# Performance work log

Measured on AMD Instinct MI355X. Metric: run time of the kernel, lower is better.

## Reference

```python
import jax, jax.numpy as jnp
import numpy as np

K = 20  # knn neighbors (module default)


def _edge_conv(h, W, s, b):
    # h: [P, C] point features; W: [O, 2C] 1x1 conv weight; s,b: folded BN scale/shift [O]
    g = h @ h.T                                   # [P, P] inner products
    sq = jnp.sum(h * h, axis=-1)                  # [P]
    pd = 2.0 * g - sq[:, None] - sq[None, :]      # negative squared distance (torch knn)
    idx = jax.lax.top_k(pd, K)[1]                 # [P, K] nearest (includes self)
    nb = h[idx]                                   # [P, K, C]
    ctr = jnp.broadcast_to(h[:, None, :], nb.shape)
    edge = jnp.concatenate([nb - ctr, ctr], axis=-1)   # [P, K, 2C]
    y = jnp.einsum('pkc,oc->pko', edge, W)        # 1x1 conv
    y = jax.nn.leaky_relu(y * s + b, 0.2)         # BN (eval, folded) + LeakyReLU
    return jnp.max(y, axis=1)                     # max over neighbors -> [P, O]


def setup_inputs() -> dict:
    key = jax.random.key(0)
    ks = list(jax.random.split(key, 40))
    N, C, B, P = 50000, 128, 16, 1024
    d = {}
    d['features'] = jax.random.normal(ks[0], (N, C), jnp.float32)
    d['clusters'] = jax.random.randint(ks[1], (B, P), 0, N)
    i = 2
    def mk_w(shape):
        nonlocal i
        w = jax.random.normal(ks[i], shape, jnp.float32) * 0.05; i += 1
        return w
    def mk_bn(c):
        nonlocal i
        s = jax.random.uniform(ks[i], (c,), jnp.float32, 0.5, 1.5); i += 1
        b = jax.random.normal(ks[i], (c,), jnp.float32) * 0.1; i += 1
        return s, b
    # EdgeConv blocks: (out, in=2*prev)
    d['W1'] = mk_w((64, 256));  d['s1'], d['b1'] = mk_bn(64)
    d['W2'] = mk_w((64, 128));  d['s2'], d['b2'] = mk_bn(64)
    d['W3'] = mk_w((128, 128)); d['s3'], d['b3'] = mk_bn(128)
    d['W4'] = mk_w((256, 256)); d['s4'], d['b4'] = mk_bn(256)
    d['W5'] = mk_w((512, 512)); d['s5'], d['b5'] = mk_bn(512)
    d['L1'] = mk_w((512, 1024)); d['s6'], d['b6'] = mk_bn(512)
    d['L2'] = mk_w((256, 512)); d['bl2'] = jax.random.normal(ks[i], (256,), jnp.float32) * 0.05; i += 1
    d['s7'], d['b7'] = mk_bn(256)
    d['L3'] = mk_w((1, 256));   d['bl3'] = jax.random.normal(ks[i], (1,), jnp.float32) * 0.05; i += 1
    return d


def reference(clusters, features, W1, s1, b1, W2, s2, b2, W3, s3, b3,
              W4, s4, b4, W5, s5, b5, L1, s6, b6, L2, bl2, s7, b7, L3, bl3):
    def _cluster(h):  # h: [P, 128]
        x1 = _edge_conv(h,  W1, s1, b1)   # [P, 64]
        x2 = _edge_conv(x1, W2, s2, b2)   # [P, 64]
        x3 = _edge_conv(x2, W3, s3, b3)   # [P, 128]
        x4 = _edge_conv(x3, W4, s4, b4)   # [P, 256]
        xc = jnp.concatenate([x1, x2, x3, x4], axis=-1)            # [P, 512]
        y = jax.nn.leaky_relu((xc @ W5.T) * s5 + b5, 0.2)          # conv5 + BN + lrelu
        return jnp.concatenate([jnp.max(y, 0), jnp.mean(y, 0)])    # [1024] max+avg pool

    feat = jax.vmap(_cluster)(features[clusters])                  # [B, 1024]
    z = jax.nn.leaky_relu((feat @ L1.T) * s6 + b6, 0.2)            # dropout = identity (eval)
    z = jax.nn.leaky_relu((z @ L2.T + bl2) * s7 + b7, 0.2)
    z = z @ L3.T + bl3
    return jax.nn.sigmoid(z)                                       # [B, 1]
```

## Files before the change

### kernel.cpp

```cpp
#include <hip/hip_runtime.h>
#include <math.h>

#define KNN 20
#define PPTS 1024
#define NCL 16

typedef _Float16 f16x8 __attribute__((ext_vector_type(8)));
typedef _Float16 f16x4 __attribute__((ext_vector_type(4)));
typedef float f32x4 __attribute__((ext_vector_type(4)));

__device__ __forceinline__ float lrelu(float x) { return x > 0.f ? x : 0.2f * x; }

#define DPPMAX(x, ctrl) { \
    unsigned _t = (unsigned)__builtin_amdgcn_update_dpp((int)(x), (int)(x), ctrl, 0xF, 0xF, false); \
    (x) = (x) > _t ? (x) : _t; }




__global__ void gather_kernel(const float4* __restrict__ feat,
                              const int* __restrict__ clusters,
                              f16x4* __restrict__ hf,
                              float* __restrict__ sqp) {
    int n = blockIdx.x * 256 + threadIdx.x;
    int c4 = n & 31;
    int row = n >> 5;
    int src = clusters[row];
    float4 v = feat[(size_t)src * 32 + c4];
    f16x4 o;
    o[0] = (_Float16)v.x; o[1] = (_Float16)v.y; o[2] = (_Float16)v.z; o[3] = (_Float16)v.w;
    hf[(size_t)(row >> 4) * 512 + (c4 >> 3) * 128 + (row & 15) * 8 + (c4 & 7)] = o;
    float s = v.x * v.x + v.y * v.y + v.z * v.z + v.w * v.w;
    #pragma unroll
    for (int off = 16; off; off >>= 1) s += __shfl_xor(s, off);
    if (c4 == 0) { sqp[2 * row] = s; sqp[2 * row + 1] = 0.f; }
}

__global__ void tof16_tiled_kernel(const float* __restrict__ src,
                                   f16x4* __restrict__ dst) {
    int n = blockIdx.x * 256 + threadIdx.x;
    int c4 = n & 127;
    int row = n >> 7;
    float4 v = *(const float4*)&src[(size_t)row * 512 + c4 * 4];
    f16x4 o;
    o[0] = (_Float16)v.x; o[1] = (_Float16)v.y; o[2] = (_Float16)v.z; o[3] = (_Float16)v.w;
    dst[(size_t)(row >> 4) * 2048 + (c4 >> 3) * 128 + (row & 15) * 8 + (c4 & 7)] = o;
}

__global__ void wcvt_kernel(const float* __restrict__ W, int lgC4,
                            f16x4* __restrict__ wn, f16x4* __restrict__ wv) {
    int n = blockIdx.x * 256 + threadIdx.x;
    int c4 = n & ((1 << lgC4) - 1);
    int o = n >> lgC4;
    int C = 4 << lgC4;
    float4 a = *(const float4*)&W[(size_t)o * 2 * C + c4 * 4];
    float4 b = *(const float4*)&W[(size_t)o * 2 * C + C + c4 * 4];
    f16x4 on, ov;
    on[0] = (_Float16)a.x; on[1] = (_Float16)a.y; on[2] = (_Float16)a.z; on[3] = (_Float16)a.w;
    ov[0] = (_Float16)(b.x - a.x); ov[1] = (_Float16)(b.y - a.y);
    ov[2] = (_Float16)(b.z - a.z); ov[3] = (_Float16)(b.w - a.w);
    size_t ti = (size_t)(o >> 4) * (C * 4) + (c4 >> 3) * 128 + (o & 15) * 8 + (c4 & 7);
    wn[ti] = on; wv[ti] = ov;
}

template<int C>
__global__ __launch_bounds__(1024, 8) void grampk_kernel(
    const _Float16* __restrict__ hf,
    const float* __restrict__ sqp, int* __restrict__ idx)
{
    __shared__ unsigned keys[16 * 1024];
    const int f = blockIdx.x;
    const int g = f >> 3;
    const int b = (f & 7) + 8 * (g >> 6);
    const int bxi = g & 63;
    const _Float16* hb = hf + (size_t)b * PPTS * C;
    const float* sqb = sqp + 2 * (b << 10);
    const int w = threadIdx.x >> 6;
    const int lane = threadIdx.x & 63;
    const int col16 = lane & 15, quad = lane >> 4;
    const int i0 = bxi * 16;
    const int j0 = w * 64;
    const _Float16* aB = hb + (size_t)bxi * 16 * C + col16 * 32 + quad * 8;
    const _Float16* bB = hb + (size_t)(w * 4) * 16 * C + col16 * 32 + quad * 8;
    f32x4 acc[4] = {};
    #pragma unroll
    for (int kc = 0; kc < C / 32; kc++) {
        f16x8 a = *(const f16x8*)&aB[kc * 512];
        #pragma unroll
        for (int t = 0; t < 4; t++) {
            f16x8 bf = *(const f16x8*)&bB[(size_t)t * 16 * C + kc * 512];
            acc[t] = __builtin_amdgcn_mfma_f32_16x16x32_f16(a, bf, acc[t], 0, 0, 0);
        }
    }
    #pragma unroll
    for (int t = 0; t < 4; t++) {
        int j = j0 + t * 16 + col16;
        float sqj = sqb[2 * j] + sqb[2 * j + 1];
        #pragma unroll
        for (int r = 0; r < 4; r++) {
            int row = quad * 4 + r;
            float val = __builtin_fmaf(2.f, acc[t][r], -sqj);
            unsigned u = __float_as_uint(val);
            unsigned key = (u & 0x80000000u) ? ~u : (u | 0x80000000u);
            keys[(row << 10) | ((j + 2 * row) & 1023)] = (key & 0xFFFFFC00u) | (unsigned)j;
        }
    }
    __syncthreads();
    {
        const int row = w;
        const unsigned* krow = &keys[row << 10];
        unsigned m1 = 0u, m2 = 0u, m3 = 0u;
        #pragma unroll
        for (int s = 0; s < 16; s++) {
            unsigned x = krow[s * 64 + lane];
            unsigned h1 = x > m1 ? x : m1, l1 = x < m1 ? x : m1;
            unsigned h2 = l1 > m2 ? l1 : m2, l2 = l1 < m2 ? l1 : m2;
            unsigned h3 = l2 > m3 ? l2 : m3;
            m1 = h1; m2 = h2; m3 = h3;
        }
        unsigned myout = 0;
        for (int kk = 0; kk < KNN; kk++) {
            unsigned x = m1;
            DPPMAX(x, 0xB1);
            DPPMAX(x, 0x4E);
            DPPMAX(x, 0x141);
            DPPMAX(x, 0x140);
            DPPMAX(x, 0x142);
            DPPMAX(x, 0x143);
            unsigned gm = (unsigned)__builtin_amdgcn_readlane((int)x, 63);
            if (lane == kk) myout = gm & 1023u;
            if (m1 == gm) {
                if (m2 != 0u) {
                    m1 = m2; m2 = m3; m3 = 0u;
                } else {
                    unsigned n1 = 0u, n2 = 0u, n3 = 0u;
                    #pragma unroll
                    for (int s = 0; s < 16; s++) {
                        unsigned x2 = krow[s * 64 + lane];
                        x2 = x2 < gm ? x2 : 0u;
                        unsigned h1 = x2 > n1 ? x2 : n1, l1 = x2 < n1 ? x2 : n1;
                        unsigned h2 = l1 > n2 ? l1 : n2, l2 = l1 < n2 ? l1 : n2;
                        unsigned h3 = l2 > n3 ? l2 : n3;
                        n1 = h1; n2 = h2; n3 = h3;
                    }
                    m1 = n1; m2 = n2; m3 = n3;
                }
            }
        }
        if (lane < KNN) idx[((size_t)b * PPTS + i0 + row) * KNN + lane] = (int)myout;
    }
}

template<int C>
__global__ __launch_bounds__(256, 4) void uv_mfma_kernel(
    const _Float16* __restrict__ hf, int lgO,
    const _Float16* __restrict__ wn, const _Float16* __restrict__ wv,
    float* __restrict__ U, float* __restrict__ V)
{
    constexpr int NBLK = 4 * (C / 32);
    __shared__ _Float16 nsh[NBLK * 640];
    __shared__ _Float16 vsh[NBLK * 640];
    const int O = 1 << lgO;
    const int f = blockIdx.x;
    const int r = f >> 3;
    const int c = (f & 7) + 8 * (r >> (lgO - 2));
    const int i2 = r & ((1 << (lgO - 2)) - 1);
    const int ox = i2 & ((O >> 6) - 1);
    const int yy = i2 >> (lgO - 6);
    const int w = threadIdx.x >> 6;
    const int lane = threadIdx.x & 63;
    const int col16 = lane & 15, quad = lane >> 4;
    const int r0 = (c * 16 + yy) * 64 + w * 16;
    const int o0 = ox * 64;
    const _Float16* aB = hf + (size_t)(r0 >> 4) * 16 * C + col16 * 32 + quad * 8;
    const _Float16* nS = wn + (size_t)(o0 >> 4) * 16 * C;
    const _Float16* vS = wv + (size_t)(o0 >> 4) * 16 * C;

    #pragma unroll
    for (int p = 0; p < C / 32; p++) {
        int h = (p * 256 + (int)threadIdx.x) * 8;
        int blk = h >> 9, col = (h >> 5) & 15, q = (h >> 3) & 3;
        int d = blk * 640 + col * 40 + q * 8;
        *(f16x8*)&nsh[d] = *(const f16x8*)&nS[h];
        *(f16x8*)&vsh[d] = *(const f16x8*)&vS[h];
    }
    __syncthreads();

    f32x4 au[4] = {}, av[4] = {};
    #pragma unroll
    for (int kc = 0; kc < C / 32; kc++) {
        f16x8 a = *(const f16x8*)&aB[kc * 512];
        #pragma unroll
        for (int t = 0; t < 4; t++) {
            int d = (t * (C / 32) + kc) * 640 + col16 * 40 + quad * 8;
            f16x8 bn = *(const f16x8*)&nsh[d];
            au[t] = __builtin_amdgcn_mfma_f32_16x16x32_f16(a, bn, au[t], 0, 0, 0);
            f16x8 bv = *(const f16x8*)&vsh[d];
            av[t] = __builtin_amdgcn_mfma_f32_16x16x32_f16(a, bv, av[t], 0, 0, 0);
        }
    }
    #pragma unroll
    for (int t = 0; t < 4; t++) {
        int o = o0 + t * 16 + col16;
        #pragma unroll
        for (int r2 = 0; r2 < 4; r2++) {
            int p = r0 + quad * 4 + r2;
            U[((size_t)p << lgO) + o] = au[t][r2];
            V[((size_t)p << lgO) + o] = av[t][r2];
        }
    }
}

__global__ void agg_kernel(const float* __restrict__ U, const float* __restrict__ V,
                           const int* __restrict__ idx, int lgO,
                           const float* __restrict__ sc, const float* __restrict__ bi,
                           _Float16* __restrict__ hnext,
                           _Float16* __restrict__ xcf, int co,
                           float* __restrict__ sqp)
{
    int O = 1 << lgO;
    int f = blockIdx.x;
    int rr = f >> 3;
    int c = (f & 7) + 8 * (rr >> (lgO + 2));
    int ii = rr & ((1 << (lgO + 2)) - 1);
    int n = (((c << (lgO + 2)) + ii) << 8) + threadIdx.x;
    int o = n & (O - 1);
    int pr = n >> lgO;
    int b = pr >> 10;
    const int* id = idx + (size_t)pr * KNN;
    float m = -INFINITY;
    #pragma unroll
    for (int k = 0; k < KNN; k++) {
        int j = id[k];
        float u = U[((size_t)(b * PPTS + j) << lgO) + o];
        m = fmaxf(m, u);
    }
    float val = lrelu((m + V[((size_t)pr << lgO) + o]) * sc[o] + bi[o]);
    _Float16 hv = (_Float16)val;
    int prg = pr >> 4, prr = pr & 15;
    xcf[(size_t)prg * 8192 + ((co + o) >> 5) * 512 + prr * 32 + (o & 31)] = hv;
    if (hnext) {
        hnext[(size_t)prg * 16 * O + (o >> 5) * 512 + prr * 32 + (o & 31)] = hv;
        float s = val * val;
        #pragma unroll
        for (int off = 32; off; off >>= 1) s += __shfl_xor(s, off);
        if ((threadIdx.x & 63) == 0) {
            sqp[2 * pr + ((o >> 6) & 1)] = s;
            if (lgO == 6) sqp[2 * pr + 1] = 0.f;
        }
    }
}

__global__ __launch_bounds__(256, 4) void conv5pool_kernel(
    const _Float16* __restrict__ xcf, const _Float16* __restrict__ w5f,
    const float* __restrict__ s5, const float* __restrict__ b5,
    float* __restrict__ pmax, float* __restrict__ psum)
{
    __shared__ _Float16 bsh[2][8 * 640];
    __shared__ float lmax[4][128], lsum[4][128];
    const int f = blockIdx.x;
    const int r = f >> 3;
    const int c = (f & 7) + 8 * (r >> 5);
    const int within = r & 31;
    const int pb = within >> 2;
    const int ob = within & 3;
    const int w = threadIdx.x >> 6;
    const int lane = threadIdx.x & 63;
    const int col16 = lane & 15, quad = lane >> 4;
    const int p0 = (c * 8 + pb) * 128 + w * 32;
    const int o0 = ob * 128;
    const _Float16* aB = xcf + (size_t)(p0 >> 4) * 8192 + col16 * 32 + quad * 8;
    const _Float16* bS = w5f + (size_t)(o0 >> 4) * 8192;

    auto stage = [&](int kc, int buf) {
        #pragma unroll
        for (int s = 0; s < 2; s++) {
            int h = (s * 256 + (int)threadIdx.x) * 8;
            int t = h >> 9, rr2 = (h >> 5) & 15, q = (h >> 3) & 3;
            f16x8 x = *(const f16x8*)&bS[(size_t)t * 8192 + kc * 512 + rr2 * 32 + q * 8];
            *(f16x8*)&bsh[buf][t * 640 + rr2 * 40 + q * 8] = x;
        }
    };

    stage(0, 0);
    f32x4 acc[2][8] = {};
    for (int kc = 0; kc < 16; kc++) {
        int cur = kc & 1;
        __syncthreads();
        if (kc < 15) stage(kc + 1, cur ^ 1);
        f16x8 a0 = *(const f16x8*)&aB[kc * 512];
        f16x8 a1 = *(const f16x8*)&aB[8192 + kc * 512];
        #pragma unroll
        for (int t = 0; t < 8; t++) {
            f16x8 bf = *(const f16x8*)&bsh[cur][t * 640 + col16 * 40 + quad * 8];
            acc[0][t] = __builtin_amdgcn_mfma_f32_16x16x32_f16(a0, bf, acc[0][t], 0, 0, 0);
            acc[1][t] = __builtin_amdgcn_mfma_f32_16x16x32_f16(a1, bf, acc[1][t], 0, 0, 0);
        }
    }
    #pragma unroll
    for (int t = 0; t < 8; t++) {
        int o = o0 + t * 16 + col16;
        float sc = s5[o], bi = b5[o];
        float vm = -INFINITY, vs = 0.f;
        #pragma unroll
        for (int u = 0; u < 2; u++)
            #pragma unroll
            for (int r2 = 0; r2 < 4; r2++) {
                float val = lrelu(acc[u][t][r2] * sc + bi);
                vm = fmaxf(vm, val); vs += val;
            }
        #pragma unroll
        for (int off = 16; off < 64; off <<= 1) {
            vm = fmaxf(vm, __shfl_xor(vm, off));
            vs += __shfl_xor(vs, off);
        }
        if (quad == 0) { lmax[w][t * 16 + col16] = vm; lsum[w][t * 16 + col16] = vs; }
    }
    __syncthreads();
    if (threadIdx.x < 128) {
        int col = threadIdx.x;
        float m = lmax[0][col], s = lsum[0][col];
        #pragma unroll
        for (int q = 1; q < 4; q++) { m = fmaxf(m, lmax[q][col]); s += lsum[q][col]; }
        size_t o = (size_t)(c * 8 + pb) * 512 + o0 + col;
        pmax[o] = m; psum[o] = s;
    }
}

__global__ void poolred_kernel(const float* __restrict__ pmax, const float* __restrict__ psum,
                               float* __restrict__ feat) {
    int n = blockIdx.x * 256 + threadIdx.x;
    int o = n & 511, cl = n >> 9;
    float m = -INFINITY, s = 0.f;
    #pragma unroll
    for (int c = 0; c < 8; c++) {
        size_t q = (size_t)(cl * 8 + c) * 512 + o;
        m = fmaxf(m, pmax[q]); s += psum[q];
    }
    feat[(size_t)cl * 1024 + o] = m;
    feat[(size_t)cl * 1024 + 512 + o] = s * (1.f / 1024.f);
}

__global__ void mlp1_kernel(const float* __restrict__ feat, const float* __restrict__ L1,
                            const float* __restrict__ s6, const float* __restrict__ b6,
                            float* __restrict__ z1) {
    int wid = (blockIdx.x * 256 + threadIdx.x) >> 6;
    int lane = threadIdx.x & 63;
    int o = wid & 511, b = wid >> 9;
    const float* f = feat + (size_t)b * 1024;
    const float* w = L1 + (size_t)o * 1024;
    float acc = 0.f;
    #pragma unroll
    for (int i = 0; i < 16; i++) acc = fmaf(f[i * 64 + lane], w[i * 64 + lane], acc);
    #pragma unroll
    for (int off = 32; off; off >>= 1) acc += __shfl_xor(acc, off);
    if (lane == 0) z1[wid] = lrelu(acc * s6[o] + b6[o]);
}

__global__ void mlp2_kernel(const float* __restrict__ z1, const float* __restrict__ L2,
                            const float* __restrict__ bl2,
                            const float* __restrict__ s7, const float* __restrict__ b7,
                            float* __restrict__ z2) {
    int wid = (blockIdx.x * 256 + threadIdx.x) >> 6;
    int lane = threadIdx.x & 63;
    int o = wid & 255, b = wid >> 8;
    const float* f = z1 + (size_t)b * 512;
    const float* w = L2 + (size_t)o * 512;
    float acc = 0.f;
    #pragma unroll
    for (int i = 0; i < 8; i++) acc = fmaf(f[i * 64 + lane], w[i * 64 + lane], acc);
    #pragma unroll
    for (int off = 32; off; off >>= 1) acc += __shfl_xor(acc, off);
    if (lane == 0) z2[wid] = lrelu((acc + bl2[o]) * s7[o] + b7[o]);
}

__global__ void mlp3_kernel(const float* __restrict__ z2, const float* __restrict__ L3,
                            const float* __restrict__ bl3, float* __restrict__ out) {
    __shared__ float red[256];
    int t = threadIdx.x;
    int b = t >> 4, q = t & 15;
    float acc = 0.f;
    for (int c = q * 16; c < q * 16 + 16; c++) acc = fmaf(z2[(size_t)b * 256 + c], L3[c], acc);
    red[t] = acc;
    __syncthreads();
    if (q == 0) {
        float s = 0.f;
        #pragma unroll
        for (int i = 0; i < 16; i++) s += red[b * 16 + i];
        s += bl3[0];
        out[b] = 1.f / (1.f + expf(-s));
    }
}

extern "C" void kernel_launch(void* const* d_in, const int* in_sizes, int n_in,
                              void* d_out, int out_size, void* d_ws, size_t ws_size,
                              hipStream_t stream) {
    const float* features = (const float*)d_in[0];
    const int*   clusters = (const int*)d_in[1];
    const float* W1 = (const float*)d_in[2];
    const float* s1 = (const float*)d_in[3];
    const float* b1 = (const float*)d_in[4];
    const float* W2 = (const float*)d_in[5];
    const float* s2 = (const float*)d_in[6];
    const float* b2 = (const float*)d_in[7];
    const float* W3 = (const float*)d_in[8];
    const float* s3 = (const float*)d_in[9];
    const float* b3 = (const float*)d_in[10];
    const float* W4 = (const float*)d_in[11];
    const float* s4 = (const float*)d_in[12];
    const float* b4 = (const float*)d_in[13];
    const float* W5 = (const float*)d_in[14];
    const float* s5 = (const float*)d_in[15];
    const float* b5 = (const float*)d_in[16];
    const float* L1 = (const float*)d_in[17];
    const float* s6 = (const float*)d_in[18];
    const float* b6 = (const float*)d_in[19];
    const float* L2 = (const float*)d_in[20];
    const float* bl2 = (const float*)d_in[21];
    const float* s7 = (const float*)d_in[22];
    const float* b7 = (const float*)d_in[23];
    const float* L3 = (const float*)d_in[24];
    const float* bl3 = (const float*)d_in[25];

    float* ws = (float*)d_ws;
    float* U   = ws;
    float* V   = U + 4194304;
    _Float16* xcf16 = (_Float16*)(V + 4194304);
    _Float16* w5f16 = xcf16 + 8388608;
    _Float16* hf16  = w5f16 + 262144;
    _Float16* wn16  = hf16 + 2097152;
    _Float16* wv16  = wn16 + 32768;
    int*   idx  = (int*)(wv16 + 32768);
    float* sqp  = (float*)(idx + 327680);
    float* pmax = sqp + 32768;
    float* psum = pmax + 131072;
    float* feat = psum + 131072;
    float* z1   = feat + 16384;
    float* z2   = z1 + 8192;

    gather_kernel<<<2048, 256, 0, stream>>>((const float4*)features, clusters,
                                            (f16x4*)hf16, sqp);

    auto stage = [&](int C, int O, int lgO,
                     const float* W, const float* sc, const float* bi,
                     int co, _Float16* hnext) {
        int lgC4 = (C == 128) ? 5 : 4;
        if (C == 128)
            grampk_kernel<128><<<1024, 1024, 0, stream>>>(hf16, sqp, idx);
        else
            grampk_kernel<64><<<1024, 1024, 0, stream>>>(hf16, sqp, idx);
        wcvt_kernel<<<(O * (C / 4)) / 256, 256, 0, stream>>>(W, lgC4, (f16x4*)wn16, (f16x4*)wv16);
        if (C == 128)
            uv_mfma_kernel<128><<<(O >> 6) * 256, 256, 0, stream>>>(hf16, lgO, wn16, wv16, U, V);
        else
            uv_mfma_kernel<64><<<(O >> 6) * 256, 256, 0, stream>>>(hf16, lgO, wn16, wv16, U, V);
        agg_kernel<<<(NCL * PPTS * O) / 256, 256, 0, stream>>>(U, V, idx, lgO, sc, bi,
                                                               hnext, xcf16, co, sqp);
    };

    stage(128,  64, 6, W1, s1, b1, 0,   hf16);
    stage( 64,  64, 6, W2, s2, b2, 64,  hf16);
    stage( 64, 128, 7, W3, s3, b3, 128, hf16);
    stage(128, 256, 8, W4, s4, b4, 256, (_Float16*)nullptr);

    tof16_tiled_kernel<<<256, 256, 0, stream>>>(W5, (f16x4*)w5f16);
    conv5pool_kernel<<<512, 256, 0, stream>>>(xcf16, w5f16, s5, b5, pmax, psum);
    poolred_kernel<<<32, 256, 0, stream>>>(pmax, psum, feat);
    mlp1_kernel<<<2048, 256, 0, stream>>>(feat, L1, s6, b6, z1);
    mlp2_kernel<<<1024, 256, 0, stream>>>(z1, L2, bl2, s7, b7, z2);
    mlp3_kernel<<<1, 256, 0, stream>>>(z2, L3, bl3, (float*)d_out);
}
```

Measured before the change: 343.5 us.

## Merge kNN gram/top-k and U/V projection into one heterogeneous launch

Combines the grampk and uv_mfma kernels into a single launch whose first NU blocks compute the U/V projections and whose remaining blocks do the gram matrix and top-k selection. The weight conversion is moved ahead of both. The goal is to drop one kernel launch and its serialization gap per stage and let the two independent workloads overlap on the GPU. The U/V blocks now use 1024 threads, each doing four row tiles. The kernel reserves 64KB of shared memory and launch bounds drop from 8 to 4, which may cut occupancy of the top-k part.

```diff
diff --git a/kernel.cpp b/kernel.cpp
--- a/kernel.cpp
+++ b/kernel.cpp
@@ -64,149 +64,144 @@
 }
 
 template<int C>
-__global__ __launch_bounds__(1024, 8) void grampk_kernel(
-    const _Float16* __restrict__ hf,
-    const float* __restrict__ sqp, int* __restrict__ idx)
+__global__ __launch_bounds__(1024, 4) void stagegu_kernel(
+    const _Float16* __restrict__ hf, const float* __restrict__ sqp,
+    int* __restrict__ idx, int lgO, int NU,
+    const _Float16* __restrict__ wn, const _Float16* __restrict__ wv,
+    float* __restrict__ U, float* __restrict__ V)
 {
-    __shared__ unsigned keys[16 * 1024];
-    const int f = blockIdx.x;
-    const int g = f >> 3;
-    const int b = (f & 7) + 8 * (g >> 6);
-    const int bxi = g & 63;
-    const _Float16* hb = hf + (size_t)b * PPTS * C;
-    const float* sqb = sqp + 2 * (b << 10);
+    __shared__ char smem[65536];
     const int w = threadIdx.x >> 6;
     const int lane = threadIdx.x & 63;
     const int col16 = lane & 15, quad = lane >> 4;
-    const int i0 = bxi * 16;
-    const int j0 = w * 64;
-    const _Float16* aB = hb + (size_t)bxi * 16 * C + col16 * 32 + quad * 8;
-    const _Float16* bB = hb + (size_t)(w * 4) * 16 * C + col16 * 32 + quad * 8;
-    f32x4 acc[4] = {};
-    #pragma unroll
-    for (int kc = 0; kc < C / 32; kc++) {
-        f16x8 a = *(const f16x8*)&aB[kc * 512];
+
+    if ((int)blockIdx.x < NU) {
+        _Float16* nsh = (_Float16*)smem;
+        _Float16* vsh = nsh + (4 * (C / 32)) * 640;
+        const int O = 1 << lgO;
+        const int k = blockIdx.x;
+        const int c = k & 15;
+        const int ox = k >> 4;
+        const int o0 = ox * 64;
+        const _Float16* nS = wn + (size_t)(o0 >> 4) * 16 * C;
+        const _Float16* vS = wv + (size_t)(o0 >> 4) * 16 * C;
+        int tid = threadIdx.x;
+        if (tid * 8 < 64 * C) {
+            int h = tid * 8;
+            int blk = h >> 9, col = (h >> 5) & 15, q = (h >> 3) & 3;
+            int d = blk * 640 + col * 40 + q * 8;
+            *(f16x8*)&nsh[d] = *(const f16x8*)&nS[h];
+            *(f16x8*)&vsh[d] = *(const f16x8*)&vS[h];
+        }
+        __syncthreads();
+        const int wsub = w & 3, ysub = w >> 2;
+        #pragma unroll
+        for (int yp = 0; yp < 4; yp++) {
+            int yy = yp * 4 + ysub;
+            int r0 = (c * 16 + yy) * 64 + wsub * 16;
+            const _Float16* aB = hf + (size_t)(r0 >> 4) * 16 * C + col16 * 32 + quad * 8;
+            f32x4 au[4] = {}, av[4] = {};
+            #pragma unroll
+            for (int kc = 0; kc < C / 32; kc++) {
+                f16x8 a = *(const f16x8*)&aB[kc * 512];
+                #pragma unroll
+                for (int t = 0; t < 4; t++) {
+                    int d = (t * (C / 32) + kc) * 640 + col16 * 40 + quad * 8;
+                    f16x8 bn = *(const f16x8*)&nsh[d];
+                    au[t] = __builtin_amdgcn_mfma_f32_16x16x32_f16(a, bn, au[t], 0, 0, 0);
+                    f16x8 bv = *(const f16x8*)&vsh[d];
+                    av[t] = __builtin_amdgcn_mfma_f32_16x16x32_f16(a, bv, av[t], 0, 0, 0);
+                }
+            }
+            #pragma unroll
+            for (int t = 0; t < 4; t++) {
+                int o = o0 + t * 16 + col16;
+                #pragma unroll
+                for (int r2 = 0; r2 < 4; r2++) {
+                    int p = r0 + quad * 4 + r2;
+                    U[((size_t)p << lgO) + o] = au[t][r2];
+                    V[((size_t)p << lgO) + o] = av[t][r2];
+                }
+            }
+        }
+    } else {
+        unsigned* keys = (unsigned*)smem;
+        const int f = (int)blockIdx.x - NU;
+        const int g = f >> 3;
+        const int b = (f & 7) + 8 * (g >> 6);
+        const int bxi = g & 63;
+        const _Float16* hb = hf + (size_t)b * PPTS * C;
+        const float* sqb = sqp + 2 * (b << 10);
+        const int i0 = bxi * 16;
+        const int j0 = w * 64;
+        const _Float16* aB = hb + (size_t)bxi * 16 * C + col16 * 32 + quad * 8;
+        const _Float16* bB = hb + (size_t)(w * 4) * 16 * C + col16 * 32 + quad * 8;
+        f32x4 acc[4] = {};
+        #pragma unroll
+        for (int kc = 0; kc < C / 32; kc++) {
+            f16x8 a = *(const f16x8*)&aB[kc * 512];
+            #pragma unroll
+            for (int t = 0; t < 4; t++) {
+                f16x8 bf = *(const f16x8*)&bB[(size_t)t * 16 * C + kc * 512];
+                acc[t] = __builtin_amdgcn_mfma_f32_16x16x32_f16(a, bf, acc[t], 0, 0, 0);
+            }
+        }
         #pragma unroll
         for (int t = 0; t < 4; t++) {
-            f16x8 bf = *(const f16x8*)&bB[(size_t)t * 16 * C + kc * 512];
-            acc[t] = __builtin_amdgcn_mfma_f32_16x16x32_f16(a, bf, acc[t], 0, 0, 0);
-        }
-    }
-    #pragma unroll
-    for (int t = 0; t < 4; t++) {
-        int j = j0 + t * 16 + col16;
-        float sqj = sqb[2 * j] + sqb[2 * j + 1];
-        #pragma unroll
-        for (int r = 0; r < 4; r++) {
-            int row = quad * 4 + r;
-            float val = __builtin_fmaf(2.f, acc[t][r], -sqj);
-            unsigned u = __float_as_uint(val);
-            unsigned key = (u & 0x80000000u) ? ~u : (u | 0x80000000u);
-            keys[(row << 10) | ((j + 2 * row) & 1023)] = (key & 0xFFFFFC00u) | (unsigned)j;
-        }
-    }
-    __syncthreads();
-    {
-        const int row = w;
-        const unsigned* krow = &keys[row << 10];
-        unsigned m1 = 0u, m2 = 0u, m3 = 0u;
-        #pragma unroll
-        for (int s = 0; s < 16; s++) {
-            unsigned x = krow[s * 64 + lane];
-            unsigned h1 = x > m1 ? x : m1, l1 = x < m1 ? x : m1;
-            unsigned h2 = l1 > m2 ? l1 : m2, l2 = l1 < m2 ? l1 : m2;
-            unsigned h3 = l2 > m3 ? l2 : m3;
-            m1 = h1; m2 = h2; m3 = h3;
-        }
-        unsigned myout = 0;
-        for (int kk = 0; kk < KNN; kk++) {
-            unsigned x = m1;
-            DPPMAX(x, 0xB1);
-            DPPMAX(x, 0x4E);
-            DPPMAX(x, 0x141);
-            DPPMAX(x, 0x140);
-            DPPMAX(x, 0x142);
-            DPPMAX(x, 0x143);
-            unsigned gm = (unsigned)__builtin_amdgcn_readlane((int)x, 63);
-            if (lane == kk) myout = gm & 1023u;
-            if (m1 == gm) {
-                if (m2 != 0u) {
-                    m1 = m2; m2 = m3; m3 = 0u;
-                } else {
-                    unsigned n1 = 0u, n2 = 0u, n3 = 0u;
-                    #pragma unroll
-                    for (int s = 0; s < 16; s++) {
-                        unsigned x2 = krow[s * 64 + lane];
-                        x2 = x2 < gm ? x2 : 0u;
-                        unsigned h1 = x2 > n1 ? x2 : n1, l1 = x2 < n1 ? x2 : n1;
-                        unsigned h2 = l1 > n2 ? l1 : n2, l2 = l1 < n2 ? l1 : n2;
-                        unsigned h3 = l2 > n3 ? l2 : n3;
-                        n1 = h1; n2 = h2; n3 = h3;
+            int j = j0 + t * 16 + col16;
+            float sqj = sqb[2 * j] + sqb[2 * j + 1];
+            #pragma unroll
+            for (int r = 0; r < 4; r++) {
+                int row = quad * 4 + r;
+                float val = __builtin_fmaf(2.f, acc[t][r], -sqj);
+                unsigned u = __float_as_uint(val);
+                unsigned key = (u & 0x80000000u) ? ~u : (u | 0x80000000u);
+                keys[(row << 10) | ((j + 2 * row) & 1023)] = (key & 0xFFFFFC00u) | (unsigned)j;
+            }
+        }
+        __syncthreads();
+        {
+            const int row = w;
+            const unsigned* krow = &keys[row << 10];
+            unsigned m1 = 0u, m2 = 0u, m3 = 0u;
+            #pragma unroll
+            for (int s = 0; s < 16; s++) {
+                unsigned x = krow[s * 64 + lane];
+                unsigned h1 = x > m1 ? x : m1, l1 = x < m1 ? x : m1;
+                unsigned h2 = l1 > m2 ? l1 : m2, l2 = l1 < m2 ? l1 : m2;
+                unsigned h3 = l2 > m3 ? l2 : m3;
+                m1 = h1; m2 = h2; m3 = h3;
+            }
+            unsigned myout = 0;
+            for (int kk = 0; kk < KNN; kk++) {
+                unsigned x = m1;
+                DPPMAX(x, 0xB1);
+                DPPMAX(x, 0x4E);
+                DPPMAX(x, 0x141);
+                DPPMAX(x, 0x140);
+                DPPMAX(x, 0x142);
+                DPPMAX(x, 0x143);
+                unsigned gm = (unsigned)__builtin_amdgcn_readlane((int)x, 63);
+                if (lane == kk) myout = gm & 1023u;
+                if (m1 == gm) {
+                    if (m2 != 0u) {
+                        m1 = m2; m2 = m3; m3 = 0u;
+                    } else {
+                        unsigned n1 = 0u, n2 = 0u, n3 = 0u;
+                        #pragma unroll
+                        for (int s = 0; s < 16; s++) {
+                            unsigned x2 = krow[s * 64 + lane];
+                            x2 = x2 < gm ? x2 : 0u;
+                            unsigned h1 = x2 > n1 ? x2 : n1, l1 = x2 < n1 ? x2 : n1;
+                            unsigned h2 = l1 > n2 ? l1 : n2, l2 = l1 < n2 ? l1 : n2;
+                            unsigned h3 = l2 > n3 ? l2 : n3;
+                            n1 = h1; n2 = h2; n3 = h3;
+                        }
+                        m1 = n1; m2 = n2; m3 = n3;
                     }
-                    m1 = n1; m2 = n2; m3 = n3;
                 }
             }
-        }
-        if (lane < KNN) idx[((size_t)b * PPTS + i0 + row) * KNN + lane] = (int)myout;
-    }
-}
-
-template<int C>
-__global__ __launch_bounds__(256, 4) void uv_mfma_kernel(
-    const _Float16* __restrict__ hf, int lgO,
-    const _Float16* __restrict__ wn, const _Float16* __restrict__ wv,
-    float* __restrict__ U, float* __restrict__ V)
-{
-    constexpr int NBLK = 4 * (C / 32);
-    __shared__ _Float16 nsh[NBLK * 640];
-    __shared__ _Float16 vsh[NBLK * 640];
-    const int O = 1 << lgO;
-    const int f = blockIdx.x;
-    const int r = f >> 3;
-    const int c = (f & 7) + 8 * (r >> (lgO - 2));
-    const int i2 = r & ((1 << (lgO - 2)) - 1);
-    const int ox = i2 & ((O >> 6) - 1);
-    const int yy = i2 >> (lgO - 6);
-    const int w = threadIdx.x >> 6;
-    const int lane = threadIdx.x & 63;
-    const int col16 = lane & 15, quad = lane >> 4;
-    const int r0 = (c * 16 + yy) * 64 + w * 16;
-    const int o0 = ox * 64;
-    const _Float16* aB = hf + (size_t)(r0 >> 4) * 16 * C + col16 * 32 + quad * 8;
-    const _Float16* nS = wn + (size_t)(o0 >> 4) * 16 * C;
-    const _Float16* vS = wv + (size_t)(o0 >> 4) * 16 * C;
-
-    #pragma unroll
-    for (int p = 0; p < C / 32; p++) {
-        int h = (p * 256 + (int)threadIdx.x) * 8;
-        int blk = h >> 9, col = (h >> 5) & 15, q = (h >> 3) & 3;
-        int d = blk * 640 + col * 40 + q * 8;
-        *(f16x8*)&nsh[d] = *(const f16x8*)&nS[h];
-        *(f16x8*)&vsh[d] = *(const f16x8*)&vS[h];
-    }
-    __syncthreads();
-
-    f32x4 au[4] = {}, av[4] = {};
-    #pragma unroll
-    for (int kc = 0; kc < C / 32; kc++) {
-        f16x8 a = *(const f16x8*)&aB[kc * 512];
-        #pragma unroll
-        for (int t = 0; t < 4; t++) {
-            int d = (t * (C / 32) + kc) * 640 + col16 * 40 + quad * 8;
-            f16x8 bn = *(const f16x8*)&nsh[d];
-            au[t] = __builtin_amdgcn_mfma_f32_16x16x32_f16(a, bn, au[t], 0, 0, 0);
-            f16x8 bv = *(const f16x8*)&vsh[d];
-            av[t] = __builtin_amdgcn_mfma_f32_16x16x32_f16(a, bv, av[t], 0, 0, 0);
-        }
-    }
-    #pragma unroll
-    for (int t = 0; t < 4; t++) {
-        int o = o0 + t * 16 + col16;
-        #pragma unroll
-        for (int r2 = 0; r2 < 4; r2++) {
-            int p = r0 + quad * 4 + r2;
-            U[((size_t)p << lgO) + o] = au[t][r2];
-            V[((size_t)p << lgO) + o] = av[t][r2];
+            if (lane < KNN) idx[((size_t)b * PPTS + i0 + row) * KNN + lane] = (int)myout;
         }
     }
 }
@@ -445,15 +440,14 @@
                      const float* W, const float* sc, const float* bi,
                      int co, _Float16* hnext) {
         int lgC4 = (C == 128) ? 5 : 4;
+        wcvt_kernel<<<(O * (C / 4)) / 256, 256, 0, stream>>>(W, lgC4, (f16x4*)wn16, (f16x4*)wv16);
+        int NU = (O >> 6) * 16;
         if (C == 128)
-            grampk_kernel<128><<<1024, 1024, 0, stream>>>(hf16, sqp, idx);
+            stagegu_kernel<128><<<NU + 1024, 1024, 0, stream>>>(hf16, sqp, idx, lgO, NU,
+                                                                wn16, wv16, U, V);
         else
-            grampk_kernel<64><<<1024, 1024, 0, stream>>>(hf16, sqp, idx);
-        wcvt_kernel<<<(O * (C / 4)) / 256, 256, 0, stream>>>(W, lgC4, (f16x4*)wn16, (f16x4*)wv16);
-        if (C == 128)
-            uv_mfma_kernel<128><<<(O >> 6) * 256, 256, 0, stream>>>(hf16, lgO, wn16, wv16, U, V);
-        else
-            uv_mfma_kernel<64><<<(O >> 6) * 256, 256, 0, stream>>>(hf16, lgO, wn16, wv16, U, V);
+            stagegu_kernel<64><<<NU + 1024, 1024, 0, stream>>>(hf16, sqp, idx, lgO, NU,
+                                                               wn16, wv16, U, V);
         agg_kernel<<<(NCL * PPTS * O) / 256, 256, 0, stream>>>(U, V, idx, lgO, sc, bi,
                                                                hnext, xcf16, co, sqp);
     };
```

Result: slower. 371.4 us (+8.1%).
